# Optimization experiments

Measured on AMD Instinct MI355X. Metric: run time of the kernel, lower is better.

Reference implementation:

```python
import jax, jax.numpy as jnp
import numpy as np

N, E, G = 50000, 800000, 256
H, C = 8, 16
F0 = 64
FH = H * C  # 128
L = 6
EPS = 1e-5
SEL = [0, 1, 2, 3, 4, 5, 5, 5]  # <10 layers -> pad with last


def setup_inputs() -> dict:
    key = jax.random.key(0)
    ks = jax.random.split(key, 32)

    def w(k, shape, fan_in):
        return jax.random.normal(k, shape, jnp.float32) / np.float32(np.sqrt(fan_in))

    inp = {
        'x': jax.random.normal(ks[0], (N, F0), jnp.float32),
        'edge_index': jax.random.randint(ks[1], (2, E), 0, N),
        'batch_vec': jnp.sort(jax.random.randint(ks[2], (N,), 0, G)),
        # layer 0 (in=F0)
        'Wq0': w(ks[3], (F0, FH), F0), 'bq0': 0.01 * jax.random.normal(ks[4], (FH,), jnp.float32),
        'Wk0': w(ks[5], (F0, FH), F0), 'bk0': 0.01 * jax.random.normal(ks[6], (FH,), jnp.float32),
        'Wv0': w(ks[7], (F0, FH), F0), 'bv0': 0.01 * jax.random.normal(ks[8], (FH,), jnp.float32),
        'Ws0': w(ks[9], (F0, FH), F0), 'bs0': 0.01 * jax.random.normal(ks[10], (FH,), jnp.float32),
        # layers 1..L-1 (in=FH), stacked
        'Wq': w(ks[11], (L - 1, FH, FH), FH), 'bq': 0.01 * jax.random.normal(ks[12], (L - 1, FH), jnp.float32),
        'Wk': w(ks[13], (L - 1, FH, FH), FH), 'bk': 0.01 * jax.random.normal(ks[14], (L - 1, FH), jnp.float32),
        'Wv': w(ks[15], (L - 1, FH, FH), FH), 'bv': 0.01 * jax.random.normal(ks[16], (L - 1, FH), jnp.float32),
        'Ws': w(ks[17], (L - 1, FH, FH), FH), 'bs': 0.01 * jax.random.normal(ks[18], (L - 1, FH), jnp.float32),
        # BatchNorm affine params per layer
        'gamma': jnp.ones((L, FH), jnp.float32),
        'beta': jnp.zeros((L, FH), jnp.float32),
    }
    return inp


def _transformer_conv(x, src, dst, Wq, bq, Wk, bk, Wv, bv, Ws, bs):
    # q from target nodes, k/v from source nodes (PyG TransformerConv, concat=True)
    q = (x @ Wq + bq).reshape(-1, H, C)
    k = (x @ Wk + bk).reshape(-1, H, C)
    v = (x @ Wv + bv).reshape(-1, H, C)
    s = jnp.einsum('ehc,ehc->eh', q[dst], k[src]) * np.float32(1.0 / np.sqrt(C))  # [E,H]
    m = jax.ops.segment_max(s, dst, num_segments=N)       # segment softmax over in-edges
    e = jnp.exp(s - m[dst])
    denom = jax.ops.segment_sum(e, dst, num_segments=N)
    alpha = e / jnp.maximum(denom[dst], 1e-16)            # [E,H]
    msg = jax.ops.segment_sum(alpha[:, :, None] * v[src], dst, num_segments=N)  # [N,H,C]
    return msg.reshape(-1, FH) + (x @ Ws + bs)            # root/skip connection


def _bn_relu(x, g, b):
    mu = jnp.mean(x, axis=0)
    var = jnp.var(x, axis=0)  # biased, as used for normalization in training mode
    return jax.nn.relu((x - mu) * jax.lax.rsqrt(var + EPS) * g + b)


def reference(x, edge_index, batch_vec, Wq0, bq0, Wk0, bk0, Wv0, bv0, Ws0, bs0,
              Wq, bq, Wk, bk, Wv, bv, Ws, bs, gamma, beta):
    src, dst = edge_index[0], edge_index[1]
    outs = []
    h = _bn_relu(_transformer_conv(x, src, dst, Wq0, bq0, Wk0, bk0, Wv0, bv0, Ws0, bs0),
                 gamma[0], beta[0])
    outs.append(h)
    for i in range(L - 1):
        h = _bn_relu(_transformer_conv(h, src, dst, Wq[i], bq[i], Wk[i], bk[i],
                                       Wv[i], bv[i], Ws[i], bs[i]),
                     gamma[i + 1], beta[i + 1])
        outs.append(h)
    counts = jnp.maximum(jax.ops.segment_sum(jnp.ones((N,), x.dtype), batch_vec, num_segments=G), 1.0)
    pooled = [jax.ops.segment_sum(o, batch_vec, num_segments=G) / counts[:, None] for o in outs]
    latent = jnp.stack([pooled[i] for i in SEL], axis=1)  # [G, 8, FH]
    return latent.reshape(G, -1)                          # [G, 8*FH]
```

## Files before the change

### kernel.cpp

```cpp
#include <hip/hip_runtime.h>
#include <hip/hip_bf16.h>
#include <math.h>

#define NN 50000
#define NE 800000
#define NG 256
#define FHH 128
#define NL 6
#define NCH 49
#define NB 391

typedef __attribute__((ext_vector_type(8))) short s16x8;
typedef __attribute__((ext_vector_type(4))) float f32x4;

#define QSCALE 0.36067376022224085f

#if defined(__has_builtin)
#if __has_builtin(__builtin_amdgcn_fdot2_f32_bf16)
#define HAVE_BFDOT 1
#endif
#endif
#ifndef HAVE_BFDOT
#define HAVE_BFDOT 0
#endif

__device__ __forceinline__ ushort f2bf(float x) {
  uint u = __float_as_uint(x);
  u += 0x7fffu + ((u >> 16) & 1u);
  return (ushort)(u >> 16);
}
__device__ __forceinline__ float bf2f(ushort h) {
  return __uint_as_float(((uint)h) << 16);
}
__device__ __forceinline__ float bfl(uint u) { return __uint_as_float(u << 16); }
__device__ __forceinline__ float bfh(uint u) { return __uint_as_float(u & 0xffff0000u); }
__device__ __forceinline__ uint packbf(float a, float b) {
  return (uint)f2bf(a) | ((uint)f2bf(b) << 16);
}

#if HAVE_BFDOT
typedef __attribute__((ext_vector_type(2))) __bf16 bf16v2;
__device__ __forceinline__ float dot2acc(uint a, uint b, float acc) {
  return __builtin_amdgcn_fdot2_f32_bf16(__builtin_bit_cast(bf16v2, a),
                                         __builtin_bit_cast(bf16v2, b), acc, false);
}
#endif

__device__ __forceinline__ void gload16(const ushort* g, ushort* l) {
  __builtin_amdgcn_global_load_lds(
      (const __attribute__((address_space(1))) uint*)(const void*)g,
      (__attribute__((address_space(3))) uint*)(void*)l, 16, 0, 0);
}

__global__ void k_gstart(const int* __restrict__ bv, int* __restrict__ gstart) {
  int g = blockIdx.x * blockDim.x + threadIdx.x;
  if (g > NG) return;
  int lo = 0, hi = NN;
  while (lo < hi) { int mid = (lo + hi) >> 1; if (bv[mid] < g) lo = mid + 1; else hi = mid; }
  gstart[g] = lo;
}

__global__ void k_deg(const int* __restrict__ dstv, int* __restrict__ deg) {
  int e = blockIdx.x * blockDim.x + threadIdx.x;
  if (e < NE) atomicAdd(&deg[dstv[e]], 1);
}

__global__ __launch_bounds__(256) void k_scanA(const int* __restrict__ deg, int* __restrict__ part) {
  int b = blockIdx.x, t = threadIdx.x;
  int s = 0;
  for (int j = t; j < 1024; j += 256) { int i = b * 1024 + j; if (i < NN) s += deg[i]; }
  __shared__ int sh[4];
  for (int o = 32; o; o >>= 1) s += __shfl_down(s, o, 64);
  if ((t & 63) == 0) sh[t >> 6] = s;
  __syncthreads();
  if (t == 0) part[b] = sh[0] + sh[1] + sh[2] + sh[3];
}

__global__ void k_scanB(int* __restrict__ part, int* __restrict__ row_ptr) {
  if (threadIdx.x == 0 && blockIdx.x == 0) {
    int run = 0;
    for (int i = 0; i < NCH; ++i) { int v = part[i]; part[i] = run; run += v; }
    row_ptr[NN] = run;
  }
}

__global__ __launch_bounds__(1024) void k_scanC(const int* __restrict__ deg, const int* __restrict__ part,
                                                int* __restrict__ row_ptr, int* __restrict__ cursor) {
  __shared__ int buf[1024];
  int b = blockIdx.x, t = threadIdx.x;
  int i = b * 1024 + t;
  int v = (i < NN) ? deg[i] : 0;
  buf[t] = v;
  __syncthreads();
  for (int off = 1; off < 1024; off <<= 1) {
    int add = (t >= off) ? buf[t - off] : 0;
    __syncthreads();
    buf[t] += add;
    __syncthreads();
  }
  if (i < NN) { int ex = part[b] + buf[t] - v; row_ptr[i] = ex; cursor[i] = ex; }
}

__global__ void k_scatter(const int* __restrict__ srcv, const int* __restrict__ dstv,
                          int* __restrict__ cursor, uint* __restrict__ colb) {
  int e = blockIdx.x * blockDim.x + threadIdx.x;
  if (e < NE) {
    int d = dstv[e];
    int pos = atomicAdd(&cursor[d], 1);
    colb[pos] = ((uint)srcv[e]) << 9;
  }
}

__device__ __forceinline__ size_t wtile_idx(int k, int c) {
  return (size_t)(k >> 5) * 4096 + ((((c >> 4) * 4 + ((k & 31) >> 3)) * 16 + (c & 15)) * 8 + (k & 7));
}

__global__ __launch_bounds__(256) void k_wconv0(const float* __restrict__ W0, const float* __restrict__ W1,
                                                const float* __restrict__ W2, const float* __restrict__ W3,
                                                ushort* __restrict__ wh, ushort* __restrict__ wl) {
  int id = blockIdx.x * 256 + threadIdx.x;
  if (id >= 4 * 64 * 128) return;
  int mat = id >> 13, rem = id & 8191;
  int k = rem >> 7, c = rem & 127;
  const float* W = (mat == 0) ? W0 : (mat == 1) ? W1 : (mat == 2) ? W2 : W3;
  float v = W[k * 128 + c];
  ushort h = f2bf(v);
  ushort lo = f2bf(v - bf2f(h));
  size_t dst = (size_t)mat * 8192 + wtile_idx(k, c);
  wh[dst] = h; wl[dst] = lo;
}

__global__ __launch_bounds__(256) void k_wconvS(const float* __restrict__ Wq, const float* __restrict__ Wk,
                                                const float* __restrict__ Wv, const float* __restrict__ Ws,
                                                ushort* __restrict__ wh, ushort* __restrict__ wl) {
  int id = blockIdx.x * 256 + threadIdx.x;
  if (id >= 5 * 4 * 16384) return;
  int lay = id / 65536, rem = id % 65536;
  int mat = rem >> 14, rem2 = rem & 16383;
  int k = rem2 >> 7, c = rem2 & 127;
  const float* W = (mat == 0) ? Wq : (mat == 1) ? Wk : (mat == 2) ? Wv : Ws;
  float v = W[(size_t)lay * 16384 + k * 128 + c];
  ushort h = f2bf(v);
  ushort lo = f2bf(v - bf2f(h));
  size_t dst = 32768 + ((size_t)lay * 4 + mat) * 16384 + wtile_idx(k, c);
  wh[dst] = h; wl[dst] = lo;
}

template <int K>
__global__ __launch_bounds__(256) void k_presplit(const float* __restrict__ Y,
                                                  ushort* __restrict__ Xh, ushort* __restrict__ Xl) {
  const int CP = K / 4;
  int idx = blockIdx.x * 256 + threadIdx.x;
  int row = idx / CP;
  int c4 = (idx % CP) * 4;
  if (row >= NN) return;
  float4 v = *reinterpret_cast<const float4*>(Y + (size_t)row * K + c4);
  ushort h0 = f2bf(v.x), h1 = f2bf(v.y), h2 = f2bf(v.z), h3 = f2bf(v.w);
  ushort l0 = f2bf(v.x - bf2f(h0)), l1 = f2bf(v.y - bf2f(h1));
  ushort l2 = f2bf(v.z - bf2f(h2)), l3 = f2bf(v.w - bf2f(h3));
  int b = row >> 7, g = (row & 127) >> 4, frow = row & 15;
  int ks = c4 >> 5, qq = (c4 & 31) >> 3, j = c4 & 7;
  size_t base = ((size_t)ks * NB + b) * 4096 + (((g * 4 + qq) * 16) + frow) * 8 + j;
  *reinterpret_cast<uint2*>(Xh + base) =
      make_uint2((uint)h0 | ((uint)h1 << 16), (uint)h2 | ((uint)h3 << 16));
  *reinterpret_cast<uint2*>(Xl + base) =
      make_uint2((uint)l0 | ((uint)l1 << 16), (uint)l2 | ((uint)l3 << 16));
}

template <int K>
__global__ __launch_bounds__(256, 2) void k_gemm(
    const ushort* __restrict__ Xh, const ushort* __restrict__ Xl,
    const ushort* __restrict__ Wth, const ushort* __restrict__ Wtl,
    const float* __restrict__ b0, const float* __restrict__ b1,
    const float* __restrict__ b2, const float* __restrict__ b3,
    ushort* __restrict__ qbf, ushort* __restrict__ kv, ushort* __restrict__ xsb) {
  __shared__ __align__(16) ushort Ah[4096];
  __shared__ __align__(16) ushort Al[4096];
  __shared__ __align__(16) ushort Bh[4096];
  __shared__ __align__(16) ushort Bl[4096];
  int bid = blockIdx.x;
  int mat = (bid >> 3) & 3;
  int b = (bid & 7) + ((bid >> 5) << 3);
  if (b >= NB) return;
  int t = threadIdx.x;
  int lane = t & 63, w = t >> 6;
  int wr = w >> 1, wc = w & 1;
  int frow = lane & 15;
  const ushort* wh = Wth + (size_t)mat * (K * 128);
  const ushort* wl = Wtl + (size_t)mat * (K * 128);
  const float* bb = (mat == 0) ? b0 : (mat == 1) ? b1 : (mat == 2) ? b2 : b3;

  f32x4 acc[4][4];
#pragma unroll
  for (int i = 0; i < 4; ++i)
#pragma unroll
    for (int j = 0; j < 4; ++j)
#pragma unroll
      for (int r = 0; r < 4; ++r) acc[i][j][r] = 0.f;

  int wofs = w * 1024 + lane * 8;
  for (int ks = 0; ks < K / 32; ++ks) {
    size_t abase = ((size_t)ks * NB + b) * 4096;
    const ushort* gAh = Xh + abase + wofs;
    const ushort* gAl = Xl + abase + wofs;
    const ushort* gBh = wh + ks * 4096 + wofs;
    const ushort* gBl = wl + ks * 4096 + wofs;
    gload16(gAh, &Ah[w * 1024]);
    gload16(gAh + 512, &Ah[w * 1024 + 512]);
    gload16(gAl, &Al[w * 1024]);
    gload16(gAl + 512, &Al[w * 1024 + 512]);
    gload16(gBh, &Bh[w * 1024]);
    gload16(gBh + 512, &Bh[w * 1024 + 512]);
    gload16(gBl, &Bl[w * 1024]);
    gload16(gBl + 512, &Bl[w * 1024 + 512]);
    __syncthreads();
    s16x8 ah[4], al[4], bh[4], bl[4];
#pragma unroll
    for (int g = 0; g < 4; ++g) {
      ah[g] = *reinterpret_cast<const s16x8*>(&Ah[(wr * 4 + g) * 512 + lane * 8]);
      al[g] = *reinterpret_cast<const s16x8*>(&Al[(wr * 4 + g) * 512 + lane * 8]);
      bh[g] = *reinterpret_cast<const s16x8*>(&Bh[(wc * 4 + g) * 512 + lane * 8]);
      bl[g] = *reinterpret_cast<const s16x8*>(&Bl[(wc * 4 + g) * 512 + lane * 8]);
    }
#pragma unroll
    for (int rg = 0; rg < 4; ++rg)
#pragma unroll
      for (int cg = 0; cg < 4; ++cg) {
        acc[rg][cg] = __builtin_amdgcn_mfma_f32_16x16x32_bf16(ah[rg], bh[cg], acc[rg][cg], 0, 0, 0);
        acc[rg][cg] = __builtin_amdgcn_mfma_f32_16x16x32_bf16(al[rg], bh[cg], acc[rg][cg], 0, 0, 0);
        acc[rg][cg] = __builtin_amdgcn_mfma_f32_16x16x32_bf16(ah[rg], bl[cg], acc[rg][cg], 0, 0, 0);
      }
    __syncthreads();
  }
  int r0 = b * 128;
  int qq = (lane >> 4) << 2;
#pragma unroll
  for (int rg = 0; rg < 4; ++rg) {
#pragma unroll
    for (int cg = 0; cg < 4; ++cg) {
      int colg = wc * 64 + cg * 16 + frow;
      float bv = bb[colg];
#pragma unroll
      for (int r = 0; r < 4; ++r) {
        int row = r0 + wr * 64 + rg * 16 + qq + r;
        if (row >= NN) continue;
        float val = acc[rg][cg][r] + bv;
        if (mat == 0)      qbf[(size_t)row * FHH + colg] = f2bf(val * QSCALE);
        else if (mat == 3) xsb[(size_t)row * FHH + colg] = f2bf(val);
        else {
          int pos = (colg >> 1) * 4 + ((mat == 2) ? 2 : 0) + (colg & 1);
          kv[(size_t)row * 256 + pos] = f2bf(val);
        }
      }
    }
  }
}

__global__ __launch_bounds__(256) void k_agg(const uint* __restrict__ qb,
                                             const ushort* __restrict__ kv,
                                             const uint* __restrict__ xsb,
                                             const int* __restrict__ row_ptr,
                                             const uint* __restrict__ colb,
                                             uint* __restrict__ yb) {
  int n = blockIdx.x * 4 + (threadIdx.x >> 6);
  int lane = threadIdx.x & 63;
  int hl = lane & 31, half = lane >> 5;
  uint2 qp = *reinterpret_cast<const uint2*>(qb + (n << 6) + 2 * hl);
#if !HAVE_BFDOT
  float qa = bfl(qp.x), qbv = bfh(qp.x), qc = bfl(qp.y), qd = bfh(qp.y);
#endif
  const char* kvb = (const char*)kv;
  uint tof = (uint)hl * 16u;
  int e0 = row_ptr[n], e1 = row_ptr[n + 1];
  float sum = 0.f, a0 = 0.f, a1 = 0.f, a2 = 0.f, a3 = 0.f;
  int i = e0;
  for (; i + 4 <= e1; i += 4) {
    uint oA = colb[i + half] + tof;
    uint oB = colb[i + 2 + half] + tof;
    uint4 dA = *(const uint4*)(kvb + oA);
    uint4 dB = *(const uint4*)(kvb + oB);
#if HAVE_BFDOT
    float pA = dot2acc(dA.z, qp.y, dot2acc(dA.x, qp.x, 0.f));
    float pB = dot2acc(dB.z, qp.y, dot2acc(dB.x, qp.x, 0.f));
#else
    float pA = qa * bfl(dA.x);
    pA = fmaf(qbv, bfh(dA.x), pA);
    pA = fmaf(qc, bfl(dA.z), pA);
    pA = fmaf(qd, bfh(dA.z), pA);
    float pB = qa * bfl(dB.x);
    pB = fmaf(qbv, bfh(dB.x), pB);
    pB = fmaf(qc, bfl(dB.z), pB);
    pB = fmaf(qd, bfh(dB.z), pB);
#endif
    pA += __shfl_xor(pA, 1, 4);  pB += __shfl_xor(pB, 1, 4);
    pA += __shfl_xor(pA, 2, 4);  pB += __shfl_xor(pB, 2, 4);
    float wA = exp2f(fminf(pA, 110.f));
    float wB = exp2f(fminf(pB, 110.f));
    sum += wA + wB;
    a0 = fmaf(wA, bfl(dA.y), fmaf(wB, bfl(dB.y), a0));
    a1 = fmaf(wA, bfh(dA.y), fmaf(wB, bfh(dB.y), a1));
    a2 = fmaf(wA, bfl(dA.w), fmaf(wB, bfl(dB.w), a2));
    a3 = fmaf(wA, bfh(dA.w), fmaf(wB, bfh(dB.w), a3));
  }
  for (; i + 2 <= e1; i += 2) {
    uint oA = colb[i + half] + tof;
    uint4 dA = *(const uint4*)(kvb + oA);
#if HAVE_BFDOT
    float pA = dot2acc(dA.z, qp.y, dot2acc(dA.x, qp.x, 0.f));
#else
    float pA = qa * bfl(dA.x);
    pA = fmaf(qbv, bfh(dA.x), pA);
    pA = fmaf(qc, bfl(dA.z), pA);
    pA = fmaf(qd, bfh(dA.z), pA);
#endif
    pA += __shfl_xor(pA, 1, 4);
    pA += __shfl_xor(pA, 2, 4);
    float wA = exp2f(fminf(pA, 110.f));
    sum += wA;
    a0 = fmaf(wA, bfl(dA.y), a0);
    a1 = fmaf(wA, bfh(dA.y), a1);
    a2 = fmaf(wA, bfl(dA.w), a2);
    a3 = fmaf(wA, bfh(dA.w), a3);
  }
  if (i < e1) {
    uint oA = colb[i] + tof;
    uint4 dA = *(const uint4*)(kvb + oA);
#if HAVE_BFDOT
    float pA = dot2acc(dA.z, qp.y, dot2acc(dA.x, qp.x, 0.f));
#else
    float pA = qa * bfl(dA.x);
    pA = fmaf(qbv, bfh(dA.x), pA);
    pA = fmaf(qc, bfl(dA.z), pA);
    pA = fmaf(qd, bfh(dA.z), pA);
#endif
    pA += __shfl_xor(pA, 1, 4);
    pA += __shfl_xor(pA, 2, 4);
    float wA = exp2f(fminf(pA, 110.f));
    if (half) wA = 0.f;
    sum += wA;
    a0 = fmaf(wA, bfl(dA.y), a0);
    a1 = fmaf(wA, bfh(dA.y), a1);
    a2 = fmaf(wA, bfl(dA.w), a2);
    a3 = fmaf(wA, bfh(dA.w), a3);
  }
  sum += __shfl_xor(sum, 32);
  a0 += __shfl_xor(a0, 32);
  a1 += __shfl_xor(a1, 32);
  a2 += __shfl_xor(a2, 32);
  a3 += __shfl_xor(a3, 32);
  float inv = 1.f / fmaxf(sum, 1e-16f);
  uint2 xv = *reinterpret_cast<const uint2*>(xsb + (n << 6) + 2 * hl);
  float o0 = fmaf(a0, inv, bfl(xv.x));
  float o1 = fmaf(a1, inv, bfh(xv.x));
  float o2 = fmaf(a2, inv, bfl(xv.y));
  float o3 = fmaf(a3, inv, bfh(xv.y));
  if (half == 0) {
    uint2 o;
    o.x = packbf(o0, o1);
    o.y = packbf(o2, o3);
    *reinterpret_cast<uint2*>(yb + (n << 6) + 2 * hl) = o;
  }
}

__global__ __launch_bounds__(256) void k_bnstats(const uint* __restrict__ yb,
                                                 float* __restrict__ stats) {
  __shared__ float2 s1[256], s2[256];
  int u = threadIdx.x & 63;
  int grp = threadIdx.x >> 6;
  float2 a = make_float2(0.f, 0.f), b = make_float2(0.f, 0.f);
  for (int r = blockIdx.x * 4 + grp; r < NN; r += 1024) {
    uint d = yb[(size_t)r * 64 + u];
    float x = bfl(d), yv = bfh(d);
    a.x += x; a.y += yv;
    b.x = fmaf(x, x, b.x); b.y = fmaf(yv, yv, b.y);
  }
  s1[threadIdx.x] = a;
  s2[threadIdx.x] = b;
  __syncthreads();
  if (grp == 0) {
#pragma unroll
    for (int g = 1; g < 4; ++g) {
      a.x += s1[u + 64 * g].x; a.y += s1[u + 64 * g].y;
      b.x += s2[u + 64 * g].x; b.y += s2[u + 64 * g].y;
    }
    atomicAdd(&stats[2 * u], a.x);
    atomicAdd(&stats[2 * u + 1], a.y);
    atomicAdd(&stats[128 + 2 * u], b.x);
    atomicAdd(&stats[128 + 2 * u + 1], b.y);
  }
}

template <int WRITE_X>
__global__ __launch_bounds__(256) void k_post(const uint* __restrict__ yb,
                                              const float* __restrict__ st,
                                              const float* __restrict__ gvec,
                                              const float* __restrict__ bvec_,
                                              const int* __restrict__ bv,
                                              const int* __restrict__ gstart,
                                              float* __restrict__ out, int layer,
                                              ushort* __restrict__ Xh, ushort* __restrict__ Xl) {
  __shared__ float acts[8][128];
  __shared__ int sg[8];
  __shared__ float ssc[128], ssh[128];
  int b = blockIdx.x, t = threadIdx.x;
  if (t < 128) {
    const float invn = 1.f / (float)NN;
    float mu = st[t] * invn;
    float var = st[128 + t] * invn - mu * mu;
    float sc = gvec[t] * rsqrtf(var + 1e-5f);
    ssc[t] = sc;
    ssh[t] = bvec_[t] - mu * sc;
  }
  if (t < 8) sg[t] = (b * 8 + t < NN) ? bv[b * 8 + t] : -1;
  __syncthreads();
  int row = b * 8 + (t >> 5);
  int c4 = (t & 31) * 4;
  bool ok = row < NN;
  float4 a = make_float4(0.f, 0.f, 0.f, 0.f);
  if (ok) {
    uint2 u2 = *reinterpret_cast<const uint2*>(yb + (size_t)row * 64 + (c4 >> 1));
    a.x = fmaxf(fmaf(bfl(u2.x), ssc[c4 + 0], ssh[c4 + 0]), 0.f);
    a.y = fmaxf(fmaf(bfh(u2.x), ssc[c4 + 1], ssh[c4 + 1]), 0.f);
    a.z = fmaxf(fmaf(bfl(u2.y), ssc[c4 + 2], ssh[c4 + 2]), 0.f);
    a.w = fmaxf(fmaf(bfh(u2.y), ssc[c4 + 3], ssh[c4 + 3]), 0.f);
  }
  *reinterpret_cast<float4*>(&acts[t >> 5][c4]) = a;
  if (WRITE_X && ok) {
    ushort h0 = f2bf(a.x), h1 = f2bf(a.y), h2 = f2bf(a.z), h3 = f2bf(a.w);
    ushort l0 = f2bf(a.x - bf2f(h0)), l1 = f2bf(a.y - bf2f(h1));
    ushort l2 = f2bf(a.z - bf2f(h2)), l3 = f2bf(a.w - bf2f(h3));
    int bb = row >> 7, g = (row & 127) >> 4, frow = row & 15;
    int ks = c4 >> 5, qq = (c4 & 31) >> 3, j = c4 & 7;
    size_t base = ((size_t)ks * NB + bb) * 4096 + (((g * 4 + qq) * 16) + frow) * 8 + j;
    *reinterpret_cast<uint2*>(Xh + base) =
        make_uint2((uint)h0 | ((uint)h1 << 16), (uint)h2 | ((uint)h3 << 16));
    *reinterpret_cast<uint2*>(Xl + base) =
        make_uint2((uint)l0 | ((uint)l1 << 16), (uint)l2 | ((uint)l3 << 16));
  }
  __syncthreads();
  if (t < 128) {
    float racc = 0.f;
    int cg = sg[0];
    for (int r = 0; r < 8; ++r) {
      int g = sg[r];
      if (g != cg) {
        if (cg >= 0) {
          float p = racc / (float)(gstart[cg + 1] - gstart[cg]);
          if (layer < 5) atomicAdd(&out[(size_t)cg * 1024 + layer * FHH + t], p);
          else {
            atomicAdd(&out[(size_t)cg * 1024 + 5 * FHH + t], p);
            atomicAdd(&out[(size_t)cg * 1024 + 6 * FHH + t], p);
            atomicAdd(&out[(size_t)cg * 1024 + 7 * FHH + t], p);
          }
        }
        racc = 0.f;
        cg = g;
      }
      racc += acts[r][t];
    }
    if (cg >= 0) {
      float p = racc / (float)(gstart[cg + 1] - gstart[cg]);
      if (layer < 5) atomicAdd(&out[(size_t)cg * 1024 + layer * FHH + t], p);
      else {
        atomicAdd(&out[(size_t)cg * 1024 + 5 * FHH + t], p);
        atomicAdd(&out[(size_t)cg * 1024 + 6 * FHH + t], p);
        atomicAdd(&out[(size_t)cg * 1024 + 7 * FHH + t], p);
      }
    }
  }
}

extern "C" void kernel_launch(void* const* d_in, const int* in_sizes, int n_in,
                              void* d_out, int out_size, void* d_ws, size_t ws_size,
                              hipStream_t stream) {
  (void)in_sizes; (void)n_in; (void)ws_size;
  const float* x    = (const float*)d_in[0];
  const int*   ei   = (const int*)d_in[1];
  const int*   bvec = (const int*)d_in[2];
  const float* Wq0  = (const float*)d_in[3];
  const float* bq0  = (const float*)d_in[4];
  const float* Wk0  = (const float*)d_in[5];
  const float* bk0  = (const float*)d_in[6];
  const float* Wv0  = (const float*)d_in[7];
  const float* bv0  = (const float*)d_in[8];
  const float* Ws0  = (const float*)d_in[9];
  const float* bs0  = (const float*)d_in[10];
  const float* WqS  = (const float*)d_in[11];
  const float* bqS  = (const float*)d_in[12];
  const float* WkS  = (const float*)d_in[13];
  const float* bkS  = (const float*)d_in[14];
  const float* WvS  = (const float*)d_in[15];
  const float* bvS  = (const float*)d_in[16];
  const float* WsS  = (const float*)d_in[17];
  const float* bsS  = (const float*)d_in[18];
  const float* gamma = (const float*)d_in[19];
  const float* beta  = (const float*)d_in[20];
  float* out = (float*)d_out;

  char* ws = (char*)d_ws;
  size_t off = 0;
  auto alloc = [&](size_t bytes) {
    void* p = ws + off;
    off = (off + bytes + 255) & ~(size_t)255;
    return p;
  };
  ushort* qbf = (ushort*)alloc((size_t)NN * FHH * 2);
  ushort* xsb = (ushort*)alloc((size_t)NN * FHH * 2);
  uint* yb    = (uint*)alloc((size_t)NN * 64 * 4);
  ushort* kv  = (ushort*)alloc((size_t)NN * 256 * 2);
  ushort* Xh  = (ushort*)alloc((size_t)4 * NB * 4096 * 2 + 8192);
  ushort* Xl  = (ushort*)alloc((size_t)4 * NB * 4096 * 2 + 8192);
  uint* colb   = (uint*)alloc((size_t)NE * 4);
  int* row_ptr = (int*)alloc((size_t)(NN + 1) * 4);
  int* cursor  = (int*)alloc((size_t)NN * 4);
  int* deg     = (int*)alloc((size_t)NN * 4);
  int* part    = (int*)alloc((size_t)NCH * 4);
  int* gstart  = (int*)alloc((size_t)(NG + 1) * 4);
  float* bstat = (float*)alloc((size_t)NL * 2 * FHH * 4);
  ushort* wsh = (ushort*)alloc((size_t)360448 * 2);
  ushort* wsl = (ushort*)alloc((size_t)360448 * 2);

  const int* srcv = ei;
  const int* dstv = ei + NE;

  hipMemsetAsync(out, 0, (size_t)out_size * 4, stream);
  hipMemsetAsync(deg, 0, (size_t)NN * 4, stream);
  hipMemsetAsync(bstat, 0, (size_t)NL * 2 * FHH * 4, stream);
  k_gstart<<<5, 64, 0, stream>>>(bvec, gstart);
  k_deg<<<(NE + 255) / 256, 256, 0, stream>>>(dstv, deg);
  k_scanA<<<NCH, 256, 0, stream>>>(deg, part);
  k_scanB<<<1, 64, 0, stream>>>(part, row_ptr);
  k_scanC<<<NCH, 1024, 0, stream>>>(deg, part, row_ptr, cursor);
  k_scatter<<<(NE + 255) / 256, 256, 0, stream>>>(srcv, dstv, cursor, colb);
  k_wconv0<<<128, 256, 0, stream>>>(Wq0, Wk0, Wv0, Ws0, wsh, wsl);
  k_wconvS<<<1280, 256, 0, stream>>>(WqS, WkS, WvS, WsS, wsh, wsl);
  k_presplit<64><<<(NN * 16 + 255) / 256, 256, 0, stream>>>(x, Xh, Xl);

  const int GEMM_GRID = 49 * 32;
  for (int l = 0; l < NL; ++l) {
    const ushort* WthL = wsh + ((l == 0) ? 0 : (size_t)32768 + (size_t)(l - 1) * 65536);
    const ushort* WtlL = wsl + ((l == 0) ? 0 : (size_t)32768 + (size_t)(l - 1) * 65536);
    const float *bq_, *bk_, *bv_, *bs_;
    if (l == 0) { bq_ = bq0; bk_ = bk0; bv_ = bv0; bs_ = bs0; }
    else {
      size_t bo = (size_t)(l - 1) * FHH;
      bq_ = bqS + bo; bk_ = bkS + bo; bv_ = bvS + bo; bs_ = bsS + bo;
    }
    if (l == 0)
      k_gemm<64><<<GEMM_GRID, 256, 0, stream>>>(Xh, Xl, WthL, WtlL, bq_, bk_, bv_, bs_, qbf, kv, xsb);
    else
      k_gemm<128><<<GEMM_GRID, 256, 0, stream>>>(Xh, Xl, WthL, WtlL, bq_, bk_, bv_, bs_, qbf, kv, xsb);
    k_agg<<<NN / 4, 256, 0, stream>>>((const uint*)qbf, kv, (const uint*)xsb, row_ptr, colb, yb);
    float* lstat = bstat + (size_t)l * 2 * FHH;
    k_bnstats<<<256, 256, 0, stream>>>(yb, lstat);
    if (l + 1 < NL)
      k_post<1><<<6250, 256, 0, stream>>>(yb, lstat, gamma + (size_t)l * FHH,
                                          beta + (size_t)l * FHH, bvec, gstart, out, l, Xh, Xl);
    else
      k_post<0><<<6250, 256, 0, stream>>>(yb, lstat, gamma + (size_t)l * FHH,
                                          beta + (size_t)l * FHH, bvec, gstart, out, l, Xh, Xl);
  }
}
```

Measured before the change: 941.4 us.

## Drop activation low-part split in GEMM and unroll edge aggregation by eight

Result: faster. 901.3 us (-4.3%).

```diff
diff --git a/kernel.cpp b/kernel.cpp
--- a/kernel.cpp
+++ b/kernel.cpp
@@ -148,7 +148,7 @@
 
 template <int K>
 __global__ __launch_bounds__(256) void k_presplit(const float* __restrict__ Y,
-                                                  ushort* __restrict__ Xh, ushort* __restrict__ Xl) {
+                                                  ushort* __restrict__ Xh) {
   const int CP = K / 4;
   int idx = blockIdx.x * 256 + threadIdx.x;
   int row = idx / CP;
@@ -156,26 +156,21 @@
   if (row >= NN) return;
   float4 v = *reinterpret_cast<const float4*>(Y + (size_t)row * K + c4);
   ushort h0 = f2bf(v.x), h1 = f2bf(v.y), h2 = f2bf(v.z), h3 = f2bf(v.w);
-  ushort l0 = f2bf(v.x - bf2f(h0)), l1 = f2bf(v.y - bf2f(h1));
-  ushort l2 = f2bf(v.z - bf2f(h2)), l3 = f2bf(v.w - bf2f(h3));
   int b = row >> 7, g = (row & 127) >> 4, frow = row & 15;
   int ks = c4 >> 5, qq = (c4 & 31) >> 3, j = c4 & 7;
   size_t base = ((size_t)ks * NB + b) * 4096 + (((g * 4 + qq) * 16) + frow) * 8 + j;
   *reinterpret_cast<uint2*>(Xh + base) =
       make_uint2((uint)h0 | ((uint)h1 << 16), (uint)h2 | ((uint)h3 << 16));
-  *reinterpret_cast<uint2*>(Xl + base) =
-      make_uint2((uint)l0 | ((uint)l1 << 16), (uint)l2 | ((uint)l3 << 16));
 }
 
 template <int K>
-__global__ __launch_bounds__(256, 2) void k_gemm(
-    const ushort* __restrict__ Xh, const ushort* __restrict__ Xl,
+__global__ __launch_bounds__(256, 3) void k_gemm(
+    const ushort* __restrict__ Xh,
     const ushort* __restrict__ Wth, const ushort* __restrict__ Wtl,
     const float* __restrict__ b0, const float* __restrict__ b1,
     const float* __restrict__ b2, const float* __restrict__ b3,
     ushort* __restrict__ qbf, ushort* __restrict__ kv, ushort* __restrict__ xsb) {
   __shared__ __align__(16) ushort Ah[4096];
-  __shared__ __align__(16) ushort Al[4096];
   __shared__ __align__(16) ushort Bh[4096];
   __shared__ __align__(16) ushort Bl[4096];
   int bid = blockIdx.x;
@@ -202,23 +197,19 @@
   for (int ks = 0; ks < K / 32; ++ks) {
     size_t abase = ((size_t)ks * NB + b) * 4096;
     const ushort* gAh = Xh + abase + wofs;
-    const ushort* gAl = Xl + abase + wofs;
     const ushort* gBh = wh + ks * 4096 + wofs;
     const ushort* gBl = wl + ks * 4096 + wofs;
     gload16(gAh, &Ah[w * 1024]);
     gload16(gAh + 512, &Ah[w * 1024 + 512]);
-    gload16(gAl, &Al[w * 1024]);
-    gload16(gAl + 512, &Al[w * 1024 + 512]);
     gload16(gBh, &Bh[w * 1024]);
     gload16(gBh + 512, &Bh[w * 1024 + 512]);
     gload16(gBl, &Bl[w * 1024]);
     gload16(gBl + 512, &Bl[w * 1024 + 512]);
     __syncthreads();
-    s16x8 ah[4], al[4], bh[4], bl[4];
+    s16x8 ah[4], bh[4], bl[4];
 #pragma unroll
     for (int g = 0; g < 4; ++g) {
       ah[g] = *reinterpret_cast<const s16x8*>(&Ah[(wr * 4 + g) * 512 + lane * 8]);
-      al[g] = *reinterpret_cast<const s16x8*>(&Al[(wr * 4 + g) * 512 + lane * 8]);
       bh[g] = *reinterpret_cast<const s16x8*>(&Bh[(wc * 4 + g) * 512 + lane * 8]);
       bl[g] = *reinterpret_cast<const s16x8*>(&Bl[(wc * 4 + g) * 512 + lane * 8]);
     }
@@ -227,7 +218,6 @@
 #pragma unroll
       for (int cg = 0; cg < 4; ++cg) {
         acc[rg][cg] = __builtin_amdgcn_mfma_f32_16x16x32_bf16(ah[rg], bh[cg], acc[rg][cg], 0, 0, 0);
-        acc[rg][cg] = __builtin_amdgcn_mfma_f32_16x16x32_bf16(al[rg], bh[cg], acc[rg][cg], 0, 0, 0);
         acc[rg][cg] = __builtin_amdgcn_mfma_f32_16x16x32_bf16(ah[rg], bl[cg], acc[rg][cg], 0, 0, 0);
       }
     __syncthreads();
@@ -274,44 +264,53 @@
   int e0 = row_ptr[n], e1 = row_ptr[n + 1];
   float sum = 0.f, a0 = 0.f, a1 = 0.f, a2 = 0.f, a3 = 0.f;
   int i = e0;
-  for (; i + 4 <= e1; i += 4) {
+#define QKDOT(d, p)                                                    \
+  {                                                                    \
+    p = qa * bfl(d.x);                                                 \
+    p = fmaf(qbv, bfh(d.x), p);                                        \
+    p = fmaf(qc, bfl(d.z), p);                                         \
+    p = fmaf(qd, bfh(d.z), p);                                         \
+  }
+  for (; i + 8 <= e1; i += 8) {
     uint oA = colb[i + half] + tof;
     uint oB = colb[i + 2 + half] + tof;
+    uint oC = colb[i + 4 + half] + tof;
+    uint oD = colb[i + 6 + half] + tof;
     uint4 dA = *(const uint4*)(kvb + oA);
     uint4 dB = *(const uint4*)(kvb + oB);
+    uint4 dC = *(const uint4*)(kvb + oC);
+    uint4 dD = *(const uint4*)(kvb + oD);
+    float pA, pB, pC, pD;
 #if HAVE_BFDOT
-    float pA = dot2acc(dA.z, qp.y, dot2acc(dA.x, qp.x, 0.f));
-    float pB = dot2acc(dB.z, qp.y, dot2acc(dB.x, qp.x, 0.f));
+    pA = dot2acc(dA.z, qp.y, dot2acc(dA.x, qp.x, 0.f));
+    pB = dot2acc(dB.z, qp.y, dot2acc(dB.x, qp.x, 0.f));
+    pC = dot2acc(dC.z, qp.y, dot2acc(dC.x, qp.x, 0.f));
+    pD = dot2acc(dD.z, qp.y, dot2acc(dD.x, qp.x, 0.f));
 #else
-    float pA = qa * bfl(dA.x);
-    pA = fmaf(qbv, bfh(dA.x), pA);
-    pA = fmaf(qc, bfl(dA.z), pA);
-    pA = fmaf(qd, bfh(dA.z), pA);
-    float pB = qa * bfl(dB.x);
-    pB = fmaf(qbv, bfh(dB.x), pB);
-    pB = fmaf(qc, bfl(dB.z), pB);
-    pB = fmaf(qd, bfh(dB.z), pB);
+    QKDOT(dA, pA) QKDOT(dB, pB) QKDOT(dC, pC) QKDOT(dD, pD)
 #endif
     pA += __shfl_xor(pA, 1, 4);  pB += __shfl_xor(pB, 1, 4);
+    pC += __shfl_xor(pC, 1, 4);  pD += __shfl_xor(pD, 1, 4);
     pA += __shfl_xor(pA, 2, 4);  pB += __shfl_xor(pB, 2, 4);
+    pC += __shfl_xor(pC, 2, 4);  pD += __shfl_xor(pD, 2, 4);
     float wA = exp2f(fminf(pA, 110.f));
     float wB = exp2f(fminf(pB, 110.f));
-    sum += wA + wB;
-    a0 = fmaf(wA, bfl(dA.y), fmaf(wB, bfl(dB.y), a0));
-    a1 = fmaf(wA, bfh(dA.y), fmaf(wB, bfh(dB.y), a1));
-    a2 = fmaf(wA, bfl(dA.w), fmaf(wB, bfl(dB.w), a2));
-    a3 = fmaf(wA, bfh(dA.w), fmaf(wB, bfh(dB.w), a3));
+    float wC = exp2f(fminf(pC, 110.f));
+    float wD = exp2f(fminf(pD, 110.f));
+    sum += (wA + wB) + (wC + wD);
+    a0 = fmaf(wA, bfl(dA.y), fmaf(wB, bfl(dB.y), fmaf(wC, bfl(dC.y), fmaf(wD, bfl(dD.y), a0))));
+    a1 = fmaf(wA, bfh(dA.y), fmaf(wB, bfh(dB.y), fmaf(wC, bfh(dC.y), fmaf(wD, bfh(dD.y), a1))));
+    a2 = fmaf(wA, bfl(dA.w), fmaf(wB, bfl(dB.w), fmaf(wC, bfl(dC.w), fmaf(wD, bfl(dD.w), a2))));
+    a3 = fmaf(wA, bfh(dA.w), fmaf(wB, bfh(dB.w), fmaf(wC, bfh(dC.w), fmaf(wD, bfh(dD.w), a3))));
   }
   for (; i + 2 <= e1; i += 2) {
     uint oA = colb[i + half] + tof;
     uint4 dA = *(const uint4*)(kvb + oA);
+    float pA;
 #if HAVE_BFDOT
-    float pA = dot2acc(dA.z, qp.y, dot2acc(dA.x, qp.x, 0.f));
+    pA = dot2acc(dA.z, qp.y, dot2acc(dA.x, qp.x, 0.f));
 #else
-    float pA = qa * bfl(dA.x);
-    pA = fmaf(qbv, bfh(dA.x), pA);
-    pA = fmaf(qc, bfl(dA.z), pA);
-    pA = fmaf(qd, bfh(dA.z), pA);
+    QKDOT(dA, pA)
 #endif
     pA += __shfl_xor(pA, 1, 4);
     pA += __shfl_xor(pA, 2, 4);
@@ -325,13 +324,11 @@
   if (i < e1) {
     uint oA = colb[i] + tof;
     uint4 dA = *(const uint4*)(kvb + oA);
+    float pA;
 #if HAVE_BFDOT
-    float pA = dot2acc(dA.z, qp.y, dot2acc(dA.x, qp.x, 0.f));
+    pA = dot2acc(dA.z, qp.y, dot2acc(dA.x, qp.x, 0.f));
 #else
-    float pA = qa * bfl(dA.x);
-    pA = fmaf(qbv, bfh(dA.x), pA);
-    pA = fmaf(qc, bfl(dA.z), pA);
-    pA = fmaf(qd, bfh(dA.z), pA);
+    QKDOT(dA, pA)
 #endif
     pA += __shfl_xor(pA, 1, 4);
     pA += __shfl_xor(pA, 2, 4);
@@ -343,6 +340,7 @@
     a2 = fmaf(wA, bfl(dA.w), a2);
     a3 = fmaf(wA, bfh(dA.w), a3);
   }
+#undef QKDOT
   sum += __shfl_xor(sum, 32);
   a0 += __shfl_xor(a0, 32);
   a1 += __shfl_xor(a1, 32);
@@ -398,7 +396,7 @@
                                               const int* __restrict__ bv,
                                               const int* __restrict__ gstart,
                                               float* __restrict__ out, int layer,
-                                              ushort* __restrict__ Xh, ushort* __restrict__ Xl) {
+                                              ushort* __restrict__ Xh) {
   __shared__ float acts[8][128];
   __shared__ int sg[8];
   __shared__ float ssc[128], ssh[128];
@@ -427,15 +425,11 @@
   *reinterpret_cast<float4*>(&acts[t >> 5][c4]) = a;
   if (WRITE_X && ok) {
     ushort h0 = f2bf(a.x), h1 = f2bf(a.y), h2 = f2bf(a.z), h3 = f2bf(a.w);
-    ushort l0 = f2bf(a.x - bf2f(h0)), l1 = f2bf(a.y - bf2f(h1));
-    ushort l2 = f2bf(a.z - bf2f(h2)), l3 = f2bf(a.w - bf2f(h3));
     int bb = row >> 7, g = (row & 127) >> 4, frow = row & 15;
     int ks = c4 >> 5, qq = (c4 & 31) >> 3, j = c4 & 7;
     size_t base = ((size_t)ks * NB + bb) * 4096 + (((g * 4 + qq) * 16) + frow) * 8 + j;
     *reinterpret_cast<uint2*>(Xh + base) =
         make_uint2((uint)h0 | ((uint)h1 << 16), (uint)h2 | ((uint)h3 << 16));
-    *reinterpret_cast<uint2*>(Xl + base) =
-        make_uint2((uint)l0 | ((uint)l1 << 16), (uint)l2 | ((uint)l3 << 16));
   }
   __syncthreads();
   if (t < 128) {
@@ -509,7 +503,6 @@
   uint* yb    = (uint*)alloc((size_t)NN * 64 * 4);
   ushort* kv  = (ushort*)alloc((size_t)NN * 256 * 2);
   ushort* Xh  = (ushort*)alloc((size_t)4 * NB * 4096 * 2 + 8192);
-  ushort* Xl  = (ushort*)alloc((size_t)4 * NB * 4096 * 2 + 8192);
   uint* colb   = (uint*)alloc((size_t)NE * 4);
   int* row_ptr = (int*)alloc((size_t)(NN + 1) * 4);
   int* cursor  = (int*)alloc((size_t)NN * 4);
@@ -534,7 +527,7 @@
   k_scatter<<<(NE + 255) / 256, 256, 0, stream>>>(srcv, dstv, cursor, colb);
   k_wconv0<<<128, 256, 0, stream>>>(Wq0, Wk0, Wv0, Ws0, wsh, wsl);
   k_wconvS<<<1280, 256, 0, stream>>>(WqS, WkS, WvS, WsS, wsh, wsl);
-  k_presplit<64><<<(NN * 16 + 255) / 256, 256, 0, stream>>>(x, Xh, Xl);
+  k_presplit<64><<<(NN * 16 + 255) / 256, 256, 0, stream>>>(x, Xh);
 
   const int GEMM_GRID = 49 * 32;
   for (int l = 0; l < NL; ++l) {
@@ -547,17 +540,17 @@
       bq_ = bqS + bo; bk_ = bkS + bo; bv_ = bvS + bo; bs_ = bsS + bo;
     }
     if (l == 0)
-      k_gemm<64><<<GEMM_GRID, 256, 0, stream>>>(Xh, Xl, WthL, WtlL, bq_, bk_, bv_, bs_, qbf, kv, xsb);
+      k_gemm<64><<<GEMM_GRID, 256, 0, stream>>>(Xh, WthL, WtlL, bq_, bk_, bv_, bs_, qbf, kv, xsb);
     else
-      k_gemm<128><<<GEMM_GRID, 256, 0, stream>>>(Xh, Xl, WthL, WtlL, bq_, bk_, bv_, bs_, qbf, kv, xsb);
+      k_gemm<128><<<GEMM_GRID, 256, 0, stream>>>(Xh, WthL, WtlL, bq_, bk_, bv_, bs_, qbf, kv, xsb);
     k_agg<<<NN / 4, 256, 0, stream>>>((const uint*)qbf, kv, (const uint*)xsb, row_ptr, colb, yb);
     float* lstat = bstat + (size_t)l * 2 * FHH;
     k_bnstats<<<256, 256, 0, stream>>>(yb, lstat);
     if (l + 1 < NL)
       k_post<1><<<6250, 256, 0, stream>>>(yb, lstat, gamma + (size_t)l * FHH,
-                                          beta + (size_t)l * FHH, bvec, gstart, out, l, Xh, Xl);
+                                          beta + (size_t)l * FHH, bvec, gstart, out, l, Xh);
     else
       k_post<0><<<6250, 256, 0, stream>>>(yb, lstat, gamma + (size_t)l * FHH,
-                                          beta + (size_t)l * FHH, bvec, gstart, out, l, Xh, Xl);
-  }
-}
+                                          beta + (size_t)l * FHH, bvec, gstart, out, l, Xh);
+  }
+}
```
